# Optimization experiments

Measured on AMD Instinct MI355X. Metric: run time of the kernel, lower is better.

The kernel has to match this reference:

```python
import jax, jax.numpy as jnp
import numpy as np
from itertools import product

SPATIAL1 = (41, 1600, 1408)  # (z,y,x) = grid[::-1] + [1,0,0]
NUM_BATCH = 2
BN_EPS = 1e-3

# ---------- numpy rulebook construction (spconv-style, done once on host) ----------

def _encode(c, shape):
    D, H, W = [int(v) for v in shape]
    return ((c[:, 0].astype(np.int64) * D + c[:, 1]) * H + c[:, 2]) * W + c[:, 3]

def _lookup(skeys, order, cand):
    pos = np.clip(np.searchsorted(skeys, cand), 0, len(skeys) - 1)
    hit = skeys[pos] == cand
    return hit, order[pos]

def _pad_rb(pairs, n_in, n_out):
    P = max(max(len(a) for a, _ in pairs), 1)
    K = len(pairs)
    ii = np.full((K, P), n_in, np.int32)   # sentinel -> zero feature row
    oo = np.full((K, P), n_out, np.int32)  # sentinel -> dummy output row
    for k, (a, b) in enumerate(pairs):
        ii[k, :len(a)] = a
        oo[k, :len(b)] = b
    return ii, oo

def _subm_rb(coords, shape):
    # SubMConv3d k=3 p=1 s=1: output sites == input sites
    N = len(coords)
    keys = _encode(coords, shape)
    order = np.argsort(keys); skeys = keys[order]
    dims = np.array(shape)
    pairs = []
    for off in product((-1, 0, 1), repeat=3):
        nb = coords[:, 1:] + np.array(off)
        ok = (nb >= 0).all(1) & (nb < dims).all(1)
        oid = np.nonzero(ok)[0]
        cand = _encode(np.concatenate([coords[ok, :1], nb[ok]], 1), shape)
        hit, iid = _lookup(skeys, order, cand)
        pairs.append((iid[hit].astype(np.int32), oid[hit].astype(np.int32)))
    return _pad_rb(pairs, N, N)

def _down_rb(coords, in_shape, ks, st, pd):
    # SparseConv3d: output site active iff any kernel tap hits an active input
    dims = np.array(in_shape); ks = np.array(ks); st = np.array(st); pd = np.array(pd)
    out_shape = (dims + 2 * pd - ks) // st + 1
    offs = list(product(*[range(int(k)) for k in ks]))
    outs = []
    for off in offs:
        o = coords[:, 1:] + pd - np.array(off)
        ok = (o % st == 0).all(1)
        od = o // st
        ok &= (od >= 0).all(1) & (od < out_shape).all(1)
        outs.append(np.concatenate([coords[ok, :1], od[ok]], 1))
    out_coords = np.unique(np.concatenate(outs, 0), axis=0)
    keys = _encode(coords, in_shape)
    order = np.argsort(keys); skeys = keys[order]
    pairs = []
    for off in offs:
        ic = out_coords[:, 1:] * st - pd + np.array(off)
        ok = (ic >= 0).all(1) & (ic < dims).all(1)
        oid = np.nonzero(ok)[0]
        cand = _encode(np.concatenate([out_coords[ok, :1], ic[ok]], 1), in_shape)
        hit, iid = _lookup(skeys, order, cand)
        pairs.append((iid[hit].astype(np.int32), oid[hit].astype(np.int32)))
    ii, oo = _pad_rb(pairs, len(coords), len(out_coords))
    return ii, oo, out_coords, tuple(int(v) for v in out_shape)

def _gen_coords(rng):
    # clustered LiDAR-like active voxels (surfaces -> local density)
    D, H, W = SPATIAL1
    per = []
    for b in range(NUM_BATCH):
        centers = rng.integers([3, 30, 30], [D - 4, H - 31, W - 31], size=(600, 3))
        pts = centers[:, None, :] + rng.integers(-3, 4, size=(600, 60, 3))
        pts = np.clip(pts.reshape(-1, 3), 0, np.array([D - 1, H - 1, W - 1]))
        uniq = np.unique(pts, axis=0)
        per.append(np.concatenate([np.full((len(uniq), 1), b, np.int64), uniq], 1))
    return np.concatenate(per, 0)

CHANS = [(27, 4, 16), (27, 16, 16), (27, 16, 32), (27, 32, 32), (27, 32, 32),
         (27, 32, 64), (27, 64, 64), (27, 64, 64), (27, 64, 64), (27, 64, 64),
         (27, 64, 64), (3, 64, 128)]

def setup_inputs() -> dict:
    rng = np.random.default_rng(0)
    coords = _gen_coords(rng)  # (N,4) [b,z,y,x]
    N = len(coords)
    s1i, s1o = _subm_rb(coords, SPATIAL1)
    d2i, d2o, c2, s2 = _down_rb(coords, SPATIAL1, (3, 3, 3), (2, 2, 2), (1, 1, 1))
    s2i, s2o = _subm_rb(c2, s2)
    d3i, d3o, c3, s3 = _down_rb(c2, s2, (3, 3, 3), (2, 2, 2), (1, 1, 1))
    s3i, s3o = _subm_rb(c3, s3)
    d4i, d4o, c4, s4 = _down_rb(c3, s3, (3, 3, 3), (2, 2, 2), (0, 1, 1))
    s4i, s4o = _subm_rb(c4, s4)
    oi, oo, c5, s5 = _down_rb(c4, s4, (3, 1, 1), (2, 1, 1), (0, 0, 0))

    key = jax.random.key(0)
    ks = jax.random.split(key, 40)
    inp = {}
    for i, (K, ci, co) in enumerate(CHANS):
        inp[f"w{i}"] = (jax.random.normal(ks[i], (K, ci, co), jnp.float32)
                         / np.sqrt(K * ci)).astype(jnp.float32)
        kb = jax.random.split(ks[12 + i], 4)
        inp[f"bn{i}"] = jnp.stack([
            jax.random.uniform(kb[0], (co,)) + 0.5,   # gamma
            jax.random.normal(kb[1], (co,)) * 0.1,    # beta
            jax.random.normal(kb[2], (co,)) * 0.1,    # running mean
            jax.random.uniform(kb[3], (co,)) + 0.5,   # running var
        ]).astype(jnp.float32)
    inp["voxels"] = jax.random.normal(ks[30], (N, 5, 4), jnp.float32)
    inp["voxel_num_points"] = jax.random.randint(ks[31], (N,), 0, 6).astype(jnp.int32)
    for name, arr in [("subm1_in", s1i), ("subm1_out", s1o), ("down2_in", d2i),
                      ("down2_out", d2o), ("subm2_in", s2i), ("subm2_out", s2o),
                      ("down3_in", d3i), ("down3_out", d3o), ("subm3_in", s3i),
                      ("subm3_out", s3o), ("down4_in", d4i), ("down4_out", d4o),
                      ("subm4_in", s4i), ("subm4_out", s4o), ("out_in", oi),
                      ("out_out", oo)]:
        inp[name] = jnp.asarray(arr)
    inp["batch_idx"] = jnp.asarray(c5[:, 0].astype(np.int32))
    inp["n2"] = len(c2); inp["n3"] = len(c3); inp["n4"] = len(c4); inp["n5"] = len(c5)
    inp["n_batch"] = NUM_BATCH
    return inp

# ---------- jax forward ----------

def _sconv(feats, w, in_idx, out_idx, n_out):
    # gather -> per-kernel-offset GEMM -> scatter-add (spconv implicit GEMM)
    fpad = jnp.concatenate([feats, jnp.zeros((1, feats.shape[1]), feats.dtype)], 0)
    g = fpad[in_idx]                                  # (K,P,Cin)
    contrib = jnp.einsum('kpi,kio->kpo', g, w)        # (K,P,Cout)
    out = jnp.zeros((n_out + 1, w.shape[2]), feats.dtype)
    return out.at[out_idx].add(contrib)[:n_out]

def _bnrelu(x, bn):
    g, b, m, v = bn  # eval-mode BatchNorm1d, eps=1e-3
    return jax.nn.relu((x - m) * jax.lax.rsqrt(v + BN_EPS) * g + b)

def reference(voxels, voxel_num_points, w0, w1, w2, w3, w4, w5, w6, w7, w8, w9,
              w10, w11, bn0, bn1, bn2, bn3, bn4, bn5, bn6, bn7, bn8, bn9, bn10,
              bn11, subm1_in, subm1_out, down2_in, down2_out, subm2_in, subm2_out,
              down3_in, down3_out, subm3_in, subm3_out, down4_in, down4_out,
              subm4_in, subm4_out, out_in, out_out, batch_idx, n2, n3, n4, n5,
              n_batch):
    # mean-VFE: average point features per voxel
    denom = jnp.maximum(voxel_num_points.astype(voxels.dtype), 1.0)[:, None]
    x = voxels.sum(1) / denom                              # (N,4)
    n1 = x.shape[0]
    x = _bnrelu(_sconv(x, w0, subm1_in, subm1_out, n1), bn0)   # conv_input
    x = _bnrelu(_sconv(x, w1, subm1_in, subm1_out, n1), bn1)   # conv1
    x = _bnrelu(_sconv(x, w2, down2_in, down2_out, n2), bn2)   # conv2 (s2)
    x = _bnrelu(_sconv(x, w3, subm2_in, subm2_out, n2), bn3)
    x = _bnrelu(_sconv(x, w4, subm2_in, subm2_out, n2), bn4)
    x = _bnrelu(_sconv(x, w5, down3_in, down3_out, n3), bn5)   # conv3 (s2)
    x = _bnrelu(_sconv(x, w6, subm3_in, subm3_out, n3), bn6)
    x = _bnrelu(_sconv(x, w7, subm3_in, subm3_out, n3), bn7)
    x = _bnrelu(_sconv(x, w8, down4_in, down4_out, n4), bn8)   # conv4 (s2)
    x = _bnrelu(_sconv(x, w9, subm4_in, subm4_out, n4), bn9)
    x = _bnrelu(_sconv(x, w10, subm4_in, subm4_out, n4), bn10)
    x = _bnrelu(_sconv(x, w11, out_in, out_out, n5), bn11)     # conv_out
    # dc_feats: per-sample global max pool over active voxels (== max_pool1d)
    dc = jax.ops.segment_max(x, batch_idx, num_segments=n_batch)
    return dc
```

## Files before the change

### kernel.cpp

```cpp
#include <hip/hip_runtime.h>

#define TPB 256
typedef unsigned short u16;
typedef __attribute__((ext_vector_type(8))) short short8v;
typedef __attribute__((ext_vector_type(4))) float f32x4;

__device__ __forceinline__ u16 f2bf(float x) {
    unsigned u = __float_as_uint(x);
    return (u16)((u + 0x7FFFu + ((u >> 16) & 1u)) >> 16);
}
__device__ __forceinline__ float bf2f(u16 h) {
    return __uint_as_float(((unsigned)h) << 16);
}

template<int CS>
__device__ __forceinline__ int swzc(int r, int c) {
    constexpr int PH = (CS == 8) ? 0 : 1;
    return c ^ ((r >> PH) & (CS - 1));
}

__device__ __forceinline__ int xcd_swz(int bid, int nwg) {
    int q = nwg >> 3, r = nwg & 7;
    int x = bid & 7, idx = bid >> 3;
    return (x < r ? x * (q + 1) : r * (q + 1) + (x - r) * q) + idx;
}

__device__ __forceinline__ void gld16(const u16* g, u16* l) {
    __builtin_amdgcn_global_load_lds(
        (const __attribute__((address_space(1))) void*)g,
        (__attribute__((address_space(3))) void*)l, 16, 0, 0);
}

__global__ void vfe_kernel(const float* __restrict__ voxels,
                           const int* __restrict__ nump,
                           float* __restrict__ x, int N) {
    int i = blockIdx.x * blockDim.x + threadIdx.x;
    if (i >= N * 4) return;
    int n = i >> 2, c = i & 3;
    const float* v = voxels + (long)n * 20 + c;
    float s = v[0] + v[4] + v[8] + v[12] + v[16];
    x[i] = s / fmaxf((float)nump[n], 1.0f);
}

__global__ void inv_build_kernel(const int* __restrict__ rb_in,
                                 const int* __restrict__ rb_out,
                                 int* __restrict__ inv,
                                 int KP, int P, int K, int n_in) {
    int t = blockIdx.x * blockDim.x + threadIdx.x;
    if (t >= KP) return;
    int ii = rb_in[t];
    if (ii == n_in) return;
    int k = t / P;
    inv[(long)rb_out[t] * K + k] = ii;
}

struct WPE { const float* w; u16* oh; u16* ol; int K, ci, co, total; };
struct WPA { WPE e[9]; };
__global__ void wprep_kernel(WPA a, int grand) {
    int t = blockIdx.x * blockDim.x + threadIdx.x;
    if (t >= grand) return;
    #pragma unroll
    for (int i = 0; i < 9; ++i) {
        if (t < a.e[i].total) {
            const WPE& E = a.e[i];
            int cc = E.ci * E.co;
            int k = t / cc, r = t % cc, c = r / E.co, o = r % E.co;
            float x = E.w[t];
            u16 h = f2bf(x);
            float lf = x - bf2f(h);
            int cs = E.ci >> 3, ph = (cs == 8) ? 0 : 1;
            int ch = c >> 3, e = c & 7;
            int sch = ch ^ ((o >> ph) & (cs - 1));
            long d = ((long)k * E.co + o) * E.ci + sch * 8 + e;
            E.oh[d] = h; E.ol[d] = f2bf(lf);
            return;
        }
        t -= a.e[i].total;
    }
}

__global__ void wprep_paired_kernel(const float* __restrict__ w,
                                    u16* __restrict__ oh, u16* __restrict__ ol,
                                    int co, int total) {
    int t = blockIdx.x * blockDim.x + threadIdx.x;
    if (t >= total) return;
    int p = t / (co * 32);
    int rem = t % (co * 32);
    int o = rem / 32, ci = rem % 32;
    int tap = 2 * p + (ci >> 4);
    float x = (tap < 27) ? w[((long)tap * 16 + (ci & 15)) * co + o] : 0.f;
    u16 h = f2bf(x);
    float lf = x - bf2f(h);
    int ch = ci >> 3, e = ci & 7;
    int sch = ch ^ ((o >> 1) & 3);
    long d = ((long)p * co + o) * 32 + sch * 8 + e;
    oh[d] = h; ol[d] = f2bf(lf);
}

template<int CO, int K>
__global__ __launch_bounds__(256)
void dconv4_kernel(const float* __restrict__ feats,
                   const float* __restrict__ w,
                   const float* __restrict__ bn,
                   const int* __restrict__ inv,
                   u16* __restrict__ oh, u16* __restrict__ ol,
                   int n_out) {
    constexpr int OG = CO / 4;
    __shared__ float sW[K * 4 * CO];
    for (int i = threadIdx.x; i < K * 4 * CO; i += 256) sW[i] = w[i];
    __syncthreads();
    long t = (long)blockIdx.x * 256 + threadIdx.x;
    int row = (int)(t / OG), og = (int)(t % OG);
    if (row >= n_out) return;
    float a0 = 0.f, a1 = 0.f, a2 = 0.f, a3 = 0.f;
    for (int k = 0; k < K; ++k) {
        int idx = inv[(long)row * K + k];
        if (idx < 0) continue;
        float4 av = *(const float4*)(feats + (long)idx * 4);
        const float* wk = sW + k * 4 * CO + og * 4;
        #pragma unroll
        for (int ci = 0; ci < 4; ++ci) {
            float a = (&av.x)[ci];
            a0 = fmaf(a, wk[ci * CO + 0], a0);
            a1 = fmaf(a, wk[ci * CO + 1], a1);
            a2 = fmaf(a, wk[ci * CO + 2], a2);
            a3 = fmaf(a, wk[ci * CO + 3], a3);
        }
    }
    float4 g = *(const float4*)(bn + og * 4);
    float4 b = *(const float4*)(bn + CO + og * 4);
    float4 m = *(const float4*)(bn + 2 * CO + og * 4);
    float4 v = *(const float4*)(bn + 3 * CO + og * 4);
    float o4[4];
    o4[0] = fmaxf((a0 - m.x) * rsqrtf(v.x + 1e-3f) * g.x + b.x, 0.f);
    o4[1] = fmaxf((a1 - m.y) * rsqrtf(v.y + 1e-3f) * g.y + b.y, 0.f);
    o4[2] = fmaxf((a2 - m.z) * rsqrtf(v.z + 1e-3f) * g.z + b.z, 0.f);
    o4[3] = fmaxf((a3 - m.w) * rsqrtf(v.w + 1e-3f) * g.w + b.w, 0.f);
    long base = (long)row * CO + og * 4;
    #pragma unroll
    for (int c = 0; c < 4; ++c) {
        u16 h = f2bf(o4[c]);
        oh[base + c] = h;
        ol[base + c] = f2bf(o4[c] - bf2f(h));
    }
}

template<int CI, int CO, int KPt, int KT, bool PAIRED, int EPI>
__global__ __launch_bounds__(256, 4)
void mconv_kernel(const u16* __restrict__ fh, const u16* __restrict__ fl,
                  const u16* __restrict__ wh, const u16* __restrict__ wl,
                  const int* __restrict__ inv,
                  const u16* __restrict__ zpage,
                  float* __restrict__ part, long slab_elems,
                  const float* __restrict__ bn,
                  u16* __restrict__ oh, u16* __restrict__ ol,
                  float* __restrict__ outf,
                  int n_out, int kpb) {
    constexpr int CS  = CI / 8;
    constexpr int LCS = (CS == 8) ? 3 : 2;
    constexpr int PH  = (CS == 8) ? 0 : 1;
    constexpr int KS  = CI / 32;
    constexpr int WC  = (CO >= 32) ? 2 : 1;
    constexpr int MT  = (WC == 2) ? 2 : 1;
    constexpr int NTW = CO / (16 * WC);
    constexpr int ASL = 64 * CS;
    constexpr int BSL = CO * CS;
    constexpr int AIT = (ASL + 255) / 256;
    constexpr int BIT = (BSL + 255) / 256;

    __shared__ __align__(16) u16 sAh[64 * CI];
    __shared__ __align__(16) u16 sAl[64 * CI];
    __shared__ __align__(16) u16 sBh[CO * CI];
    __shared__ __align__(16) u16 sBl[CO * CI];

    const int t = threadIdx.x;
    const int bx = xcd_swz(blockIdx.x, gridDim.x);
    const int brow = bx * 64;
    const int kbeg = blockIdx.y * kpb;
    const int kend = (kbeg + kpb < KPt) ? (kbeg + kpb) : KPt;

    const int lane = t & 63, wid = t >> 6;
    const int wr = wid / WC, wc = wid % WC;
    const int frow = lane & 15;
    const int fch  = lane >> 4;

    f32x4 acc[MT][NTW];
    #pragma unroll
    for (int mt = 0; mt < MT; ++mt)
        #pragma unroll
        for (int nt = 0; nt < NTW; ++nt) {
            acc[mt][nt][0] = 0.f; acc[mt][nt][1] = 0.f;
            acc[mt][nt][2] = 0.f; acc[mt][nt][3] = 0.f;
        }

    auto stage = [&](int k) {
        #pragma unroll
        for (int s = 0; s < AIT; ++s) {
            int slot = s * 256 + t;
            if (ASL % 256 == 0 || slot < ASL) {
                int r = slot >> LCS, cc = slot & (CS - 1);
                int c = cc ^ ((r >> PH) & (CS - 1));
                int grow = brow + r;
                const u16 *srcH, *srcL;
                if (PAIRED) {
                    int tap = 2 * k + (c >> 1);
                    int idx = (grow < n_out && tap < KT)
                              ? inv[(long)grow * KT + tap] : -1;
                    srcH = (idx >= 0) ? fh + (long)idx * 16 + (c & 1) * 8 : zpage;
                    srcL = (idx >= 0) ? fl + (long)idx * 16 + (c & 1) * 8 : zpage;
                } else {
                    int idx = (grow < n_out) ? inv[(long)grow * KT + k] : -1;
                    srcH = (idx >= 0) ? fh + (long)idx * CI + c * 8 : zpage;
                    srcL = (idx >= 0) ? fl + (long)idx * CI + c * 8 : zpage;
                }
                gld16(srcH, sAh + (s * 256 + wid * 64) * 8);
                gld16(srcL, sAl + (s * 256 + wid * 64) * 8);
            }
        }
        const u16* gbh = wh + (long)k * CO * CI;
        const u16* gbl = wl + (long)k * CO * CI;
        #pragma unroll
        for (int s = 0; s < BIT; ++s) {
            int slot = s * 256 + t;
            if (BSL % 256 == 0 || slot < BSL) {
                gld16(gbh + (long)slot * 8, sBh + (s * 256 + wid * 64) * 8);
                gld16(gbl + (long)slot * 8, sBl + (s * 256 + wid * 64) * 8);
            }
        }
    };
    auto compute = [&]() {
        #pragma unroll
        for (int ks = 0; ks < KS; ++ks) {
            int c = ks * 4 + fch;
            short8v ah[MT], al[MT];
            #pragma unroll
            for (int mt = 0; mt < MT; ++mt) {
                int r = wr * (MT * 16) + mt * 16 + frow;
                int o = r * CI + swzc<CS>(r, c) * 8;
                ah[mt] = *(const short8v*)(sAh + o);
                al[mt] = *(const short8v*)(sAl + o);
            }
            #pragma unroll
            for (int nt = 0; nt < NTW; ++nt) {
                int col = wc * (CO / WC) + nt * 16 + frow;
                int o = col * CI + swzc<CS>(col, c) * 8;
                short8v bh = *(const short8v*)(sBh + o);
                short8v bl = *(const short8v*)(sBl + o);
                #pragma unroll
                for (int mt = 0; mt < MT; ++mt) {
                    acc[mt][nt] = __builtin_amdgcn_mfma_f32_16x16x32_bf16(ah[mt], bh, acc[mt][nt], 0, 0, 0);
                    acc[mt][nt] = __builtin_amdgcn_mfma_f32_16x16x32_bf16(ah[mt], bl, acc[mt][nt], 0, 0, 0);
                    acc[mt][nt] = __builtin_amdgcn_mfma_f32_16x16x32_bf16(al[mt], bh, acc[mt][nt], 0, 0, 0);
                }
            }
        }
    };

    for (int k = kbeg; k < kend; ++k) {
        stage(k);
        __syncthreads();
        compute();
        if (k + 1 < kend) __syncthreads();
    }

    if constexpr (EPI == 0) {
        float* dst = part + (long)blockIdx.y * slab_elems;
        #pragma unroll
        for (int mt = 0; mt < MT; ++mt) {
            int orow0 = brow + wr * (MT * 16) + mt * 16 + (lane >> 4) * 4;
            #pragma unroll
            for (int nt = 0; nt < NTW; ++nt) {
                int ocol = wc * (CO / WC) + nt * 16 + (lane & 15);
                #pragma unroll
                for (int j = 0; j < 4; ++j) {
                    int r = orow0 + j;
                    if (r < n_out) dst[(long)r * CO + ocol] = acc[mt][nt][j];
                }
            }
        }
    } else {
        #pragma unroll
        for (int mt = 0; mt < MT; ++mt) {
            int orow0 = brow + wr * (MT * 16) + mt * 16 + (lane >> 4) * 4;
            #pragma unroll
            for (int nt = 0; nt < NTW; ++nt) {
                int ocol = wc * (CO / WC) + nt * 16 + (lane & 15);
                float g = bn[ocol], bb = bn[CO + ocol];
                float m = bn[2 * CO + ocol], vv = bn[3 * CO + ocol];
                float sc = rsqrtf(vv + 1e-3f) * g;
                #pragma unroll
                for (int j = 0; j < 4; ++j) {
                    int r = orow0 + j;
                    if (r < n_out) {
                        float yv = fmaxf((acc[mt][nt][j] - m) * sc + bb, 0.f);
                        if constexpr (EPI == 1) {
                            u16 h = f2bf(yv);
                            oh[(long)r * CO + ocol] = h;
                            ol[(long)r * CO + ocol] = f2bf(yv - bf2f(h));
                        } else {
                            outf[(long)r * CO + ocol] = yv;
                        }
                    }
                }
            }
        }
    }
}

template<bool EMIT16>
__global__ void reduce_bnrelu_kernel(const float* __restrict__ part, long stride,
                                     int ys, const float* __restrict__ bn, int co,
                                     float* __restrict__ outf,
                                     u16* __restrict__ oh, u16* __restrict__ ol,
                                     long total) {
    long t = (long)blockIdx.x * blockDim.x + threadIdx.x;
    if (t >= total) return;
    float s = 0.f;
    for (int y = 0; y < ys; ++y) s += part[(long)y * stride + t];
    int o = (int)(t % co);
    float g = bn[o], b = bn[co + o], m = bn[2 * co + o], v = bn[3 * co + o];
    float yv = fmaxf((s - m) * rsqrtf(v + 1e-3f) * g + b, 0.f);
    if (EMIT16) {
        u16 h = f2bf(yv);
        oh[t] = h;
        ol[t] = f2bf(yv - bf2f(h));
    } else {
        outf[t] = yv;
    }
}

__global__ void segmax_kernel(const float* __restrict__ x,
                              const int* __restrict__ bidx,
                              float* __restrict__ out, int rows, int nb) {
    __shared__ float sM[8 * 128];
    for (int i = threadIdx.x; i < nb * 128; i += 256) sM[i] = 0.f;
    __syncthreads();
    int c = threadIdx.x & 127;
    int sub = threadIdx.x >> 7;
    for (int r = blockIdx.x * 2 + sub; r < rows; r += gridDim.x * 2) {
        float v = x[(long)r * 128 + c];
        int b = bidx[r];
        atomicMax((int*)&sM[b * 128 + c], __float_as_int(v));
    }
    __syncthreads();
    for (int i = threadIdx.x; i < nb * 128; i += 256)
        atomicMax((int*)out + i, __float_as_int(sM[i]));
}

extern "C" void kernel_launch(void* const* d_in, const int* in_sizes, int n_in,
                              void* d_out, int out_size, void* d_ws, size_t ws_size,
                              hipStream_t stream) {
    (void)n_in;
    const float* voxels = (const float*)d_in[24];
    const int*   nump   = (const int*)d_in[25];
    const int N  = in_sizes[25];
    const int n2 = in_sizes[30] / 27;
    const int n3 = in_sizes[34] / 27;
    const int n4 = in_sizes[38] / 27;
    const int n5 = in_sizes[42];

    struct L { int wi, rb, K, ci, co, nin, nout; };
    const L layers[12] = {
        {0,  26, 27,  4,  16, N,  N }, {1,  26, 27, 16,  16, N,  N },
        {2,  28, 27, 16,  32, N,  n2}, {3,  30, 27, 32,  32, n2, n2},
        {4,  30, 27, 32,  32, n2, n2}, {5,  32, 27, 32,  64, n2, n3},
        {6,  34, 27, 64,  64, n3, n3}, {7,  34, 27, 64,  64, n3, n3},
        {8,  36, 27, 64,  64, n3, n4}, {9,  38, 27, 64,  64, n4, n4},
        {10, 38, 27, 64,  64, n4, n4}, {11, 40,  3, 64, 128, n4, n5},
    };
    struct RBD { int rb, K, nin, nout; };
    const RBD rbs[8] = {
        {26, 27, N,  N }, {28, 27, N,  n2}, {30, 27, n2, n2}, {32, 27, n2, n3},
        {34, 27, n3, n3}, {36, 27, n3, n4}, {38, 27, n4, n4}, {40, 3,  n4, n5},
    };
    const int invmap[12] = {0, 0, 1, 2, 2, 3, 4, 4, 5, 6, 6, 7};

    size_t feat_elems = (size_t)N * 4, wt_elems = 0, arena_elems = 0;
    for (int i = 0; i < 12; ++i) {
        size_t fe = (size_t)layers[i].nout * layers[i].co;
        if (fe > feat_elems) feat_elems = fe;
        if (i >= 3) wt_elems += (size_t)layers[i].K * layers[i].ci * layers[i].co;
    }
    for (int r = 0; r < 8; ++r) arena_elems += (size_t)rbs[r].nout * rbs[r].K;
    const size_t wp1_elems = 14 * 32 * 16;
    const size_t wp2_elems = 14 * 32 * 32;
    auto al = [](size_t x) { return (x + 255) & ~(size_t)255; };
    char* p = (char*)d_ws;
    u16*   zpage = (u16*)p; p += 256;
    int*   inv_arena = (int*)p; p += al(arena_elems * 4);
    float* bufA = (float*)p; p += al(feat_elems * 4);
    u16* ph[2]; u16* pl[2];
    ph[0] = (u16*)p; p += al(feat_elems * 2);
    pl[0] = (u16*)p; p += al(feat_elems * 2);
    ph[1] = (u16*)p; p += al(feat_elems * 2);
    pl[1] = (u16*)p; p += al(feat_elems * 2);
    u16* wth = (u16*)p; p += al(wt_elems * 2);
    u16* wtl = (u16*)p; p += al(wt_elems * 2);
    u16* wp1h = (u16*)p; p += al(wp1_elems * 2);
    u16* wp1l = (u16*)p; p += al(wp1_elems * 2);
    u16* wp2h = (u16*)p; p += al(wp2_elems * 2);
    u16* wp2l = (u16*)p; p += al(wp2_elems * 2);
    float* slab = (float*)p;
    size_t slab_budget = ws_size - (size_t)((char*)slab - (char*)d_ws);

    hipMemsetAsync(zpage, 0, 256, stream);

    int* invs[8];
    {
        size_t off = 0;
        for (int r = 0; r < 8; ++r) { invs[r] = inv_arena + off; off += (size_t)rbs[r].nout * rbs[r].K; }
        hipMemsetAsync(inv_arena, 0xFF, arena_elems * sizeof(int), stream);
        for (int r = 0; r < 8; ++r) {
            const int* rin  = (const int*)d_in[rbs[r].rb];
            const int* rout = (const int*)d_in[rbs[r].rb + 1];
            int P  = in_sizes[rbs[r].rb] / rbs[r].K;
            int KP = rbs[r].K * P;
            inv_build_kernel<<<dim3((KP + TPB - 1) / TPB), dim3(TPB), 0, stream>>>(
                rin, rout, invs[r], KP, P, rbs[r].K, rbs[r].nin);
        }
    }

    {
        long tot = (long)N * 4;
        vfe_kernel<<<dim3((unsigned)((tot + TPB - 1) / TPB)), dim3(TPB), 0, stream>>>(
            voxels, nump, bufA, N);
    }

    size_t woff[9];
    {
        WPA wa;
        size_t off = 0;
        for (int i = 0; i < 9; ++i) {
            const L& l = layers[i + 3];
            woff[i] = off;
            wa.e[i].w  = (const float*)d_in[2 * l.wi];
            wa.e[i].oh = wth + off;
            wa.e[i].ol = wtl + off;
            wa.e[i].K = l.K; wa.e[i].ci = l.ci; wa.e[i].co = l.co;
            wa.e[i].total = l.K * l.ci * l.co;
            off += (size_t)wa.e[i].total;
        }
        int grand = (int)off;
        wprep_kernel<<<dim3((grand + TPB - 1) / TPB), dim3(TPB), 0, stream>>>(wa, grand);
        wprep_paired_kernel<<<dim3(((int)wp1_elems + TPB - 1) / TPB), dim3(TPB), 0, stream>>>(
            (const float*)d_in[2], wp1h, wp1l, 16, (int)wp1_elems);
        wprep_paired_kernel<<<dim3(((int)wp2_elems + TPB - 1) / TPB), dim3(TPB), 0, stream>>>(
            (const float*)d_in[4], wp2h, wp2l, 32, (int)wp2_elems);
    }

    {
        const L& l = layers[0];
        long tot = (long)l.nout * 4;
        dconv4_kernel<16, 27><<<dim3((unsigned)((tot + 255) / 256)), 256, 0, stream>>>(
            bufA, (const float*)d_in[0], (const float*)d_in[1], invs[0],
            ph[0], pl[0], l.nout);
    }

    int cset = 0;
    for (int i = 1; i < 12; ++i) {
        const L& l = layers[i];
        const int* invp = invs[invmap[i]];
        unsigned blocks = (unsigned)((l.nout + 63) / 64);
        int KPv = (i <= 2) ? 14 : l.K;
        int ysmax = (KPv == 14) ? 9 : ((KPv == 27) ? 27 : 3);
        size_t per = (size_t)l.nout * l.co * 4;
        int ys = 1;
        while (ys < ysmax && blocks * (unsigned)ys < 768) ys *= 3;
        if (ys > ysmax) ys = ysmax;
        while (ys > 1 && (size_t)ys * per > slab_budget) ys /= 3;
        int kpb = (KPv + ys - 1) / ys;
        long slab_elems = (long)l.nout * l.co;
        dim3 grid(blocks, (unsigned)ys);
        const float* bn = (const float*)d_in[2 * l.wi + 1];
        const u16* fh = ph[cset];
        const u16* fl = pl[cset];
        const u16* whp = (i >= 3) ? wth + woff[i - 3] : nullptr;
        const u16* wlp = (i >= 3) ? wtl + woff[i - 3] : nullptr;

        #define MCONV(CI_, CO_, KP_, KT_, PRD_, WH_, WL_)                              \
            do {                                                                       \
                if (ys == 1 && i < 11)                                                 \
                    mconv_kernel<CI_, CO_, KP_, KT_, PRD_, 1><<<grid, 256, 0, stream>>>( \
                        fh, fl, WH_, WL_, invp, zpage, nullptr, 0, bn,                 \
                        ph[cset ^ 1], pl[cset ^ 1], nullptr, l.nout, kpb);             \
                else if (ys == 1)                                                      \
                    mconv_kernel<CI_, CO_, KP_, KT_, PRD_, 2><<<grid, 256, 0, stream>>>( \
                        fh, fl, WH_, WL_, invp, zpage, nullptr, 0, bn,                 \
                        nullptr, nullptr, bufA, l.nout, kpb);                          \
                else                                                                   \
                    mconv_kernel<CI_, CO_, KP_, KT_, PRD_, 0><<<grid, 256, 0, stream>>>( \
                        fh, fl, WH_, WL_, invp, zpage, slab, slab_elems, bn,           \
                        nullptr, nullptr, nullptr, l.nout, kpb);                       \
            } while (0)

        switch (i) {
        case 1:          MCONV(32, 16, 14, 27, true,  wp1h, wp1l); break;
        case 2:          MCONV(32, 32, 14, 27, true,  wp2h, wp2l); break;
        case 3: case 4:  MCONV(32, 32, 27, 27, false, whp, wlp);   break;
        case 5:          MCONV(32, 64, 27, 27, false, whp, wlp);   break;
        case 11:         MCONV(64, 128, 3, 3,  false, whp, wlp);   break;
        default:         MCONV(64, 64, 27, 27, false, whp, wlp);   break;
        }
        #undef MCONV

        if (ys == 1) {
            if (i < 11) cset ^= 1;
        } else {
            long total = (long)l.nout * l.co;
            unsigned rblocks = (unsigned)((total + TPB - 1) / TPB);
            if (i < 11) {
                reduce_bnrelu_kernel<true><<<dim3(rblocks), dim3(TPB), 0, stream>>>(
                    slab, slab_elems, ys, bn, l.co,
                    nullptr, ph[cset ^ 1], pl[cset ^ 1], total);
                cset ^= 1;
            } else {
                reduce_bnrelu_kernel<false><<<dim3(rblocks), dim3(TPB), 0, stream>>>(
                    slab, slab_elems, ys, bn, l.co, bufA, nullptr, nullptr, total);
            }
        }
    }

    hipMemsetAsync(d_out, 0, (size_t)out_size * sizeof(float), stream);
    const int* bidx = (const int*)d_in[42];
    int nb = out_size / 128;
    segmax_kernel<<<dim3(128), dim3(256), 0, stream>>>(bufA, bidx, (float*)d_out, n5, nb);
}
```

Before: 432.2 us.

## Use 128-row tiles for 64-channel sparse conv layers and batch setup kernels

New measurement: 471.5 us. 9.1% more time.

```diff
diff --git a/kernel.cpp b/kernel.cpp
--- a/kernel.cpp
+++ b/kernel.cpp
@@ -42,59 +42,63 @@
     x[i] = s / fmaxf((float)nump[n], 1.0f);
 }
 
-__global__ void inv_build_kernel(const int* __restrict__ rb_in,
-                                 const int* __restrict__ rb_out,
-                                 int* __restrict__ inv,
-                                 int KP, int P, int K, int n_in) {
-    int t = blockIdx.x * blockDim.x + threadIdx.x;
-    if (t >= KP) return;
-    int ii = rb_in[t];
-    if (ii == n_in) return;
-    int k = t / P;
-    inv[(long)rb_out[t] * K + k] = ii;
-}
-
-struct WPE { const float* w; u16* oh; u16* ol; int K, ci, co, total; };
-struct WPA { WPE e[9]; };
-__global__ void wprep_kernel(WPA a, int grand) {
-    int t = blockIdx.x * blockDim.x + threadIdx.x;
+struct IBE { const int* rin; const int* rout; int* inv; int P, K, n_in, KP; };
+struct IBA { IBE e[8]; };
+__global__ void inv_build_all_kernel(IBA a, long grand) {
+    long t = (long)blockIdx.x * blockDim.x + threadIdx.x;
     if (t >= grand) return;
     #pragma unroll
-    for (int i = 0; i < 9; ++i) {
+    for (int i = 0; i < 8; ++i) {
+        if (t < a.e[i].KP) {
+            const IBE& E = a.e[i];
+            int ii = E.rin[t];
+            if (ii != E.n_in) {
+                int k = (int)(t / E.P);
+                E.inv[(long)E.rout[t] * E.K + k] = ii;
+            }
+            return;
+        }
+        t -= a.e[i].KP;
+    }
+}
+
+struct WPE { const float* w; u16* oh; u16* ol; int K, ci, co, total, paired; };
+struct WPA { WPE e[11]; };
+__global__ void wprep_kernel(WPA a, long grand) {
+    long t = (long)blockIdx.x * blockDim.x + threadIdx.x;
+    if (t >= grand) return;
+    #pragma unroll
+    for (int i = 0; i < 11; ++i) {
         if (t < a.e[i].total) {
             const WPE& E = a.e[i];
-            int cc = E.ci * E.co;
-            int k = t / cc, r = t % cc, c = r / E.co, o = r % E.co;
-            float x = E.w[t];
-            u16 h = f2bf(x);
-            float lf = x - bf2f(h);
-            int cs = E.ci >> 3, ph = (cs == 8) ? 0 : 1;
-            int ch = c >> 3, e = c & 7;
-            int sch = ch ^ ((o >> ph) & (cs - 1));
-            long d = ((long)k * E.co + o) * E.ci + sch * 8 + e;
-            E.oh[d] = h; E.ol[d] = f2bf(lf);
+            if (E.paired) {
+                int p = (int)(t / (E.co * 32));
+                int rem = (int)(t % (E.co * 32));
+                int o = rem / 32, ci = rem % 32;
+                int tap = 2 * p + (ci >> 4);
+                float x = (tap < 27) ? E.w[((long)tap * 16 + (ci & 15)) * E.co + o] : 0.f;
+                u16 h = f2bf(x);
+                float lf = x - bf2f(h);
+                int ch = ci >> 3, e = ci & 7;
+                int sch = ch ^ ((o >> 1) & 3);
+                long d = ((long)p * E.co + o) * 32 + sch * 8 + e;
+                E.oh[d] = h; E.ol[d] = f2bf(lf);
+            } else {
+                int cc = E.ci * E.co;
+                int k = (int)(t / cc), r = (int)(t % cc), c = r / E.co, o = r % E.co;
+                float x = E.w[t];
+                u16 h = f2bf(x);
+                float lf = x - bf2f(h);
+                int cs = E.ci >> 3, ph = (cs == 8) ? 0 : 1;
+                int ch = c >> 3, e = c & 7;
+                int sch = ch ^ ((o >> ph) & (cs - 1));
+                long d = ((long)k * E.co + o) * E.ci + sch * 8 + e;
+                E.oh[d] = h; E.ol[d] = f2bf(lf);
+            }
             return;
         }
         t -= a.e[i].total;
     }
-}
-
-__global__ void wprep_paired_kernel(const float* __restrict__ w,
-                                    u16* __restrict__ oh, u16* __restrict__ ol,
-                                    int co, int total) {
-    int t = blockIdx.x * blockDim.x + threadIdx.x;
-    if (t >= total) return;
-    int p = t / (co * 32);
-    int rem = t % (co * 32);
-    int o = rem / 32, ci = rem % 32;
-    int tap = 2 * p + (ci >> 4);
-    float x = (tap < 27) ? w[((long)tap * 16 + (ci & 15)) * co + o] : 0.f;
-    u16 h = f2bf(x);
-    float lf = x - bf2f(h);
-    int ch = ci >> 3, e = ci & 7;
-    int sch = ch ^ ((o >> 1) & 3);
-    long d = ((long)p * co + o) * 32 + sch * 8 + e;
-    oh[d] = h; ol[d] = f2bf(lf);
 }
 
 template<int CO, int K>
@@ -145,7 +149,7 @@
     }
 }
 
-template<int CI, int CO, int KPt, int KT, bool PAIRED, int EPI>
+template<int CI, int CO, int ROWS, int KPt, int KT, bool PAIRED, int EPI>
 __global__ __launch_bounds__(256, 4)
 void mconv_kernel(const u16* __restrict__ fh, const u16* __restrict__ fl,
                   const u16* __restrict__ wh, const u16* __restrict__ wl,
@@ -160,22 +164,23 @@
     constexpr int LCS = (CS == 8) ? 3 : 2;
     constexpr int PH  = (CS == 8) ? 0 : 1;
     constexpr int KS  = CI / 32;
-    constexpr int WC  = (CO >= 32) ? 2 : 1;
-    constexpr int MT  = (WC == 2) ? 2 : 1;
+    constexpr int WC  = (ROWS == 128) ? 1 : ((CO >= 32) ? 2 : 1);
+    constexpr int WRW = 4 / WC;
+    constexpr int MT  = ROWS / (16 * WRW);
     constexpr int NTW = CO / (16 * WC);
-    constexpr int ASL = 64 * CS;
+    constexpr int ASL = ROWS * CS;
     constexpr int BSL = CO * CS;
     constexpr int AIT = (ASL + 255) / 256;
     constexpr int BIT = (BSL + 255) / 256;
 
-    __shared__ __align__(16) u16 sAh[64 * CI];
-    __shared__ __align__(16) u16 sAl[64 * CI];
+    __shared__ __align__(16) u16 sAh[ROWS * CI];
+    __shared__ __align__(16) u16 sAl[ROWS * CI];
     __shared__ __align__(16) u16 sBh[CO * CI];
     __shared__ __align__(16) u16 sBl[CO * CI];
 
     const int t = threadIdx.x;
     const int bx = xcd_swz(blockIdx.x, gridDim.x);
-    const int brow = bx * 64;
+    const int brow = bx * ROWS;
     const int kbeg = blockIdx.y * kpb;
     const int kend = (kbeg + kpb < KPt) ? (kbeg + kpb) : KPt;
 
@@ -374,6 +379,7 @@
         {34, 27, n3, n3}, {36, 27, n3, n4}, {38, 27, n4, n4}, {40, 3,  n4, n5},
     };
     const int invmap[12] = {0, 0, 1, 2, 2, 3, 4, 4, 5, 6, 6, 7};
+    const int rowsv[12]  = {64, 64, 64, 64, 64, 128, 128, 128, 128, 128, 128, 64};
 
     size_t feat_elems = (size_t)N * 4, wt_elems = 0, arena_elems = 0;
     for (int i = 0; i < 12; ++i) {
@@ -410,14 +416,18 @@
         size_t off = 0;
         for (int r = 0; r < 8; ++r) { invs[r] = inv_arena + off; off += (size_t)rbs[r].nout * rbs[r].K; }
         hipMemsetAsync(inv_arena, 0xFF, arena_elems * sizeof(int), stream);
+        IBA ia;
+        long grand = 0;
         for (int r = 0; r < 8; ++r) {
-            const int* rin  = (const int*)d_in[rbs[r].rb];
-            const int* rout = (const int*)d_in[rbs[r].rb + 1];
             int P  = in_sizes[rbs[r].rb] / rbs[r].K;
-            int KP = rbs[r].K * P;
-            inv_build_kernel<<<dim3((KP + TPB - 1) / TPB), dim3(TPB), 0, stream>>>(
-                rin, rout, invs[r], KP, P, rbs[r].K, rbs[r].nin);
-        }
+            ia.e[r].rin  = (const int*)d_in[rbs[r].rb];
+            ia.e[r].rout = (const int*)d_in[rbs[r].rb + 1];
+            ia.e[r].inv  = invs[r];
+            ia.e[r].P = P; ia.e[r].K = rbs[r].K; ia.e[r].n_in = rbs[r].nin;
+            ia.e[r].KP = rbs[r].K * P;
+            grand += ia.e[r].KP;
+        }
+        inv_build_all_kernel<<<dim3((unsigned)((grand + TPB - 1) / TPB)), dim3(TPB), 0, stream>>>(ia, grand);
     }
 
     {
@@ -438,14 +448,13 @@
             wa.e[i].ol = wtl + off;
             wa.e[i].K = l.K; wa.e[i].ci = l.ci; wa.e[i].co = l.co;
             wa.e[i].total = l.K * l.ci * l.co;
+            wa.e[i].paired = 0;
             off += (size_t)wa.e[i].total;
         }
-        int grand = (int)off;
-        wprep_kernel<<<dim3((grand + TPB - 1) / TPB), dim3(TPB), 0, stream>>>(wa, grand);
-        wprep_paired_kernel<<<dim3(((int)wp1_elems + TPB - 1) / TPB), dim3(TPB), 0, stream>>>(
-            (const float*)d_in[2], wp1h, wp1l, 16, (int)wp1_elems);
-        wprep_paired_kernel<<<dim3(((int)wp2_elems + TPB - 1) / TPB), dim3(TPB), 0, stream>>>(
-            (const float*)d_in[4], wp2h, wp2l, 32, (int)wp2_elems);
+        wa.e[9]  = { (const float*)d_in[2], wp1h, wp1l, 27, 16, 16, (int)wp1_elems, 1 };
+        wa.e[10] = { (const float*)d_in[4], wp2h, wp2l, 27, 16, 32, (int)wp2_elems, 1 };
+        long grand = (long)off + wp1_elems + wp2_elems;
+        wprep_kernel<<<dim3((unsigned)((grand + TPB - 1) / TPB)), dim3(TPB), 0, stream>>>(wa, grand);
     }
 
     {
@@ -460,7 +469,8 @@
     for (int i = 1; i < 12; ++i) {
         const L& l = layers[i];
         const int* invp = invs[invmap[i]];
-        unsigned blocks = (unsigned)((l.nout + 63) / 64);
+        int ROWS = rowsv[i];
+        unsigned blocks = (unsigned)((l.nout + ROWS - 1) / ROWS);
         int KPv = (i <= 2) ? 14 : l.K;
         int ysmax = (KPv == 14) ? 9 : ((KPv == 27) ? 27 : 3);
         size_t per = (size_t)l.nout * l.co * 4;
@@ -477,29 +487,29 @@
         const u16* whp = (i >= 3) ? wth + woff[i - 3] : nullptr;
         const u16* wlp = (i >= 3) ? wtl + woff[i - 3] : nullptr;
 
-        #define MCONV(CI_, CO_, KP_, KT_, PRD_, WH_, WL_)                              \
+        #define MCONV(CI_, CO_, RW_, KP_, KT_, PRD_, WH_, WL_)                         \
             do {                                                                       \
                 if (ys == 1 && i < 11)                                                 \
-                    mconv_kernel<CI_, CO_, KP_, KT_, PRD_, 1><<<grid, 256, 0, stream>>>( \
+                    mconv_kernel<CI_, CO_, RW_, KP_, KT_, PRD_, 1><<<grid, 256, 0, stream>>>( \
                         fh, fl, WH_, WL_, invp, zpage, nullptr, 0, bn,                 \
                         ph[cset ^ 1], pl[cset ^ 1], nullptr, l.nout, kpb);             \
                 else if (ys == 1)                                                      \
-                    mconv_kernel<CI_, CO_, KP_, KT_, PRD_, 2><<<grid, 256, 0, stream>>>( \
+                    mconv_kernel<CI_, CO_, RW_, KP_, KT_, PRD_, 2><<<grid, 256, 0, stream>>>( \
                         fh, fl, WH_, WL_, invp, zpage, nullptr, 0, bn,                 \
                         nullptr, nullptr, bufA, l.nout, kpb);                          \
                 else                                                                   \
-                    mconv_kernel<CI_, CO_, KP_, KT_, PRD_, 0><<<grid, 256, 0, stream>>>( \
+                    mconv_kernel<CI_, CO_, RW_, KP_, KT_, PRD_, 0><<<grid, 256, 0, stream>>>( \
                         fh, fl, WH_, WL_, invp, zpage, slab, slab_elems, bn,           \
                         nullptr, nullptr, nullptr, l.nout, kpb);                       \
             } while (0)
 
         switch (i) {
-        case 1:          MCONV(32, 16, 14, 27, true,  wp1h, wp1l); break;
-        case 2:          MCONV(32, 32, 14, 27, true,  wp2h, wp2l); break;
-        case 3: case 4:  MCONV(32, 32, 27, 27, false, whp, wlp);   break;
-        case 5:          MCONV(32, 64, 27, 27, false, whp, wlp);   break;
-        case 11:         MCONV(64, 128, 3, 3,  false, whp, wlp);   break;
-        default:         MCONV(64, 64, 27, 27, false, whp, wlp);   break;
+        case 1:          MCONV(32, 16, 64, 14, 27, true,  wp1h, wp1l); break;
+        case 2:          MCONV(32, 32, 64, 14, 27, true,  wp2h, wp2l); break;
+        case 3: case 4:  MCONV(32, 32, 64, 27, 27, false, whp, wlp);   break;
+        case 5:          MCONV(32, 64, 128, 27, 27, false, whp, wlp);  break;
+        case 11:         MCONV(64, 128, 64, 3, 3,  false, whp, wlp);   break;
+        default:         MCONV(64, 64, 128, 27, 27, false, whp, wlp);  break;
         }
         #undef MCONV
 
```
